# Optimization experiments

Measured on AMD Instinct MI355X. Metric: run time of the kernel, lower is better.

The kernel has to match this reference:

```python
import jax, jax.numpy as jnp
import numpy as np

DIM = 1024
NUM_HEADS = 16
HEAD_DIM = DIM // NUM_HEADS
SCALE = HEAD_DIM ** -0.5


def setup_inputs() -> dict:
    key = jax.random.key(0)
    k_x, k_wqkv, k_bqkv, k_wp, k_bp = jax.random.split(key, 5)
    B, C, D = 4, 1024, DIM
    x = jax.random.normal(k_x, (B, C, D), dtype=jnp.float32)
    # nn.Linear stores weight as (out, in); we keep (in, out) for x @ W
    w_qkv = jax.random.normal(k_wqkv, (D, 3 * D), dtype=jnp.float32) * (D ** -0.5)
    b_qkv = jax.random.normal(k_bqkv, (3 * D,), dtype=jnp.float32) * 0.02
    w_proj = jax.random.normal(k_wp, (D, D), dtype=jnp.float32) * (D ** -0.5)
    b_proj = jax.random.normal(k_bp, (D,), dtype=jnp.float32) * 0.02
    return {"x": x, "w_qkv": w_qkv, "b_qkv": b_qkv, "w_proj": w_proj, "b_proj": b_proj}


def reference(x, w_qkv, b_qkv, w_proj, b_proj):
    B, C, D = x.shape
    H, Hd = NUM_HEADS, HEAD_DIM
    qkv = x @ w_qkv + b_qkv                       # (B, C, 3D)
    qkv = qkv.reshape(B, C, 3, H, Hd)
    q = qkv[:, :, 0].transpose(0, 2, 1, 3)        # (B, H, C, Hd)
    k = qkv[:, :, 1].transpose(0, 2, 1, 3)
    v = qkv[:, :, 2].transpose(0, 2, 1, 3)
    attn = jnp.einsum('bhqd,bhkd->bhqk', q, k) * SCALE
    attn = jax.nn.softmax(attn, axis=-1)
    out = jnp.einsum('bhqk,bhkd->bhqd', attn, v)  # (B, H, C, Hd)
    out = out.transpose(0, 2, 1, 3).reshape(B, C, D)
    return out @ w_proj + b_proj
```

## Files before the change

kernel.cpp:

```cpp
#include <hip/hip_runtime.h>
#include <cstdint>

#define BB 4
#define CC 1024
#define DD 1024
#define HH 16
#define HD 64
#define NH3 3072

typedef __attribute__((ext_vector_type(8))) short short8;
typedef __attribute__((ext_vector_type(4))) float f32x4;

#define MFMA16(a, b, c) __builtin_amdgcn_mfma_f32_16x16x32_bf16(a, b, c, 0, 0, 0)
#define EXP2 __builtin_amdgcn_exp2f

__device__ __forceinline__ void glds16(const void* g, void* l) {
    __builtin_amdgcn_global_load_lds(
        (const __attribute__((address_space(1))) void*)g,
        (__attribute__((address_space(3))) void*)l, 16, 0, 0);
}

__device__ __forceinline__ ushort f2bf(float f) {
    union { float f; uint32_t u; } v; v.f = f;
    uint32_t r = v.u + 0x7FFF + ((v.u >> 16) & 1);
    return (ushort)(r >> 16);
}

__device__ __forceinline__ uint32_t pack2bf(float a, float b) {
    uint32_t ua = __float_as_uint(a), ub = __float_as_uint(b);
    ua += 0x7FFF + ((ua >> 16) & 1);
    ub += 0x7FFF + ((ub >> 16) & 1);
    return __builtin_amdgcn_perm(ua, ub, 0x03020706);
}

__global__ __launch_bounds__(256)
void prep_kernel(const float* __restrict__ x, ushort* __restrict__ xbf,
                 const float* __restrict__ wqkv, ushort* __restrict__ wqkvT,
                 const float* __restrict__ wprj, ushort* __restrict__ wprjT)
{
    __shared__ float Ts[64 * 65];
    const int blk = blockIdx.x;
    const int t = threadIdx.x;

    if (blk < 4096) {
        int i = blk * 256 + t;
        float4 v = ((const float4*)x)[i];
        ushort4 o;
        o.x = f2bf(v.x); o.y = f2bf(v.y); o.z = f2bf(v.z); o.w = f2bf(v.w);
        ((ushort4*)xbf)[i] = o;
        return;
    }

    const float* in; ushort* outp; int K, N, n0, k0;
    if (blk < 4864) {
        int bx = blk - 4096;
        in = wqkv; outp = wqkvT; K = DD; N = NH3;
        n0 = (bx % 48) * 64; k0 = (bx / 48) * 64;
    } else {
        int bx = blk - 4864;
        in = wprj; outp = wprjT; K = DD; N = DD;
        n0 = (bx % 16) * 64; k0 = (bx / 16) * 64;
    }
    #pragma unroll
    for (int i = 0; i < 16; ++i) {
        int idx = t + i * 256;
        int r = idx >> 6, c = idx & 63;
        Ts[r * 65 + c] = in[(size_t)(k0 + r) * N + n0 + c];
    }
    __syncthreads();
    #pragma unroll
    for (int i = 0; i < 16; ++i) {
        int idx = t + i * 256;
        int rr = idx >> 6, cc = idx & 63;
        outp[(size_t)(n0 + rr) * K + k0 + cc] = f2bf(Ts[cc * 65 + rr]);
    }
}

template<int MODE, int MT>
__global__ __launch_bounds__(256)
void gemm_bt(const ushort* __restrict__ A, const ushort* __restrict__ Bt,
             const float* __restrict__ bias, float* __restrict__ Cf,
             ushort* __restrict__ qb, ushort* __restrict__ kb, ushort* __restrict__ vtb,
             int M, int N, int K)
{
    constexpr int MI = MT / 32;
    __shared__ ushort As[3][MT * 32];
    __shared__ ushort Bs[3][128 * 32];

    const int tid = threadIdx.x;
    const int wid = tid >> 6, lane = tid & 63;
    const int quad = lane >> 4, l15 = lane & 15;
    const int m0 = blockIdx.y * MT, n0 = blockIdx.x * 128;
    const int wm = (wid >> 1) * (MT / 2), wn = (wid & 1) * 64;

    const int sr = lane >> 2;
    const int sc = lane & 3;

    const int ar0 = wid * (MT / 4) + sr;
    const int acg0 = sc ^ ((ar0 >> 1) & 3);
    const int acg1 = sc ^ (((ar0 + 16) >> 1) & 3);
    const ushort* Ar0 = A + (size_t)(m0 + ar0) * K + acg0 * 8;
    const ushort* Ar1 = A + (size_t)(m0 + ar0 + 16) * K + acg1 * 8;
    const int br0 = wid * 32 + sr;
    const int bcg0 = sc ^ ((br0 >> 1) & 3);
    const int bcg1 = sc ^ (((br0 + 16) >> 1) & 3);
    const ushort* Br0 = Bt + (size_t)(n0 + br0) * K + bcg0 * 8;
    const ushort* Br1 = Bt + (size_t)(n0 + br0 + 16) * K + bcg1 * 8;

    f32x4 acc[MI][4];
    #pragma unroll
    for (int i = 0; i < MI; ++i)
        #pragma unroll
        for (int j = 0; j < 4; ++j) acc[i][j] = (f32x4)(0.0f);

#define GSTAGE(kn, bidx) do { \
        glds16(Ar0 + (kn), &As[bidx][(wid * (MT / 4)) * 32]); \
        glds16(Br0 + (kn), &Bs[bidx][(wid * 32) * 32]); \
        if (MT == 128) glds16(Ar1 + (kn), &As[bidx][(wid * 32 + 16) * 32]); \
        glds16(Br1 + (kn), &Bs[bidx][(wid * 32 + 16) * 32]); } while (0)

    GSTAGE(0, 0);
    GSTAGE(32, 1);

    int cur = 0;
    for (int k0 = 0; k0 < K; k0 += 32) {
        if (k0 + 32 < K) {
            if (MT == 128)
                asm volatile("s_waitcnt vmcnt(4)\n\ts_barrier" ::: "memory");
            else
                asm volatile("s_waitcnt vmcnt(3)\n\ts_barrier" ::: "memory");
        } else {
            asm volatile("s_waitcnt vmcnt(0)\n\ts_barrier" ::: "memory");
        }
        if (k0 + 64 < K) {
            const int nb = (cur >= 1) ? cur - 1 : 2;
            GSTAGE(k0 + 64, nb);
        }

        short8 af[MI], bf[4];
        #pragma unroll
        for (int i = 0; i < MI; ++i) {
            int row = wm + i * 16 + l15;
            af[i] = *(const short8*)(&As[cur][row * 32 + (quad ^ ((row >> 1) & 3)) * 8]);
        }
        #pragma unroll
        for (int j = 0; j < 4; ++j) {
            int col = wn + j * 16 + l15;
            bf[j] = *(const short8*)(&Bs[cur][col * 32 + (quad ^ ((col >> 1) & 3)) * 8]);
        }
        #pragma unroll
        for (int i = 0; i < MI; ++i)
            #pragma unroll
            for (int j = 0; j < 4; ++j)
                acc[i][j] = MFMA16(af[i], bf[j], acc[i][j]);

        cur = (cur == 2) ? 0 : cur + 1;
    }
#undef GSTAGE

    if (MODE == 0) {
        #pragma unroll
        for (int i = 0; i < MI; ++i) {
            int row = m0 + wm + i * 16 + quad * 4;
            #pragma unroll
            for (int j = 0; j < 4; ++j) {
                int col = n0 + wn + j * 16 + l15;
                float bv = bias[col];
                #pragma unroll
                for (int r = 0; r < 4; ++r)
                    Cf[(size_t)(row + r) * N + col] = acc[i][j][r] + bv;
            }
        }
    } else {
        #pragma unroll
        for (int j = 0; j < 4; ++j) {
            int n = n0 + wn + j * 16 + l15;
            int three = n >> 10;
            int h = (n >> 6) & 15;
            int hd = n & 63;
            float scale = (three == 0) ? 0.1803368801f : 1.0f;
            float bv = bias[n];
            #pragma unroll
            for (int i = 0; i < MI; ++i) {
                int row = m0 + wm + i * 16 + quad * 4;
                #pragma unroll
                for (int r = 0; r < 4; ++r) {
                    int m = row + r;
                    int b = m >> 10, c = m & 1023;
                    ushort val = f2bf((acc[i][j][r] + bv) * scale);
                    if (three == 0)
                        qb[((size_t)((b * HH + h) * CC) + c) * HD + hd] = val;
                    else if (three == 1)
                        kb[((size_t)((b * HH + h) * CC) + c) * HD + hd] = val;
                    else
                        vtb[((size_t)((b * HH + h) * HD) + hd) * CC + c] = val;
                }
            }
        }
    }
}

__global__ __launch_bounds__(256)
void attn_mfma6(const ushort* __restrict__ qb, const ushort* __restrict__ kb,
                const ushort* __restrict__ vt, ushort* __restrict__ attnb)
{
    __shared__ ushort lds[2 * 4096 + 3 * 4096 + 2 * 9216];
    const uint K0 = 0, K1 = 4096;
    const uint V0 = 8192, V1 = 12288, V2 = 16384;
    const uint P0 = 20480, P1 = 29696;

    const int tid = threadIdx.x;
    const int wid = tid >> 6, lane = tid & 63;
    const int quad = lane >> 4, l15 = lane & 15;
    const int bh = blockIdx.x & 63;
    const int qt = blockIdx.x >> 6;
    const int q0 = qt * 128;
    const int b = bh >> 4, h = bh & 15;

    const ushort* Qp  = qb + ((size_t)bh * CC + q0) * HD;
    const ushort* Kp  = kb + (size_t)bh * CC * HD;
    const ushort* Vtp = vt + (size_t)bh * HD * CC;

    const int sr = lane >> 3;
    const int sc = lane & 7;

    short8 qf[2][2];
    #pragma unroll
    for (int q2 = 0; q2 < 2; ++q2) {
        int row = wid * 32 + q2 * 16 + l15;
        #pragma unroll
        for (int s = 0; s < 2; ++s)
            qf[q2][s] = *(const short8*)(Qp + (size_t)row * HD + (s * 4 + quad) * 8);
    }

    const int kr = wid * 16 + sr;
    const int cgA = sc ^ (kr & 7);
    const int cgB = sc ^ ((kr + 8) & 7);
    const ushort* Kr0 = Kp  + (size_t)kr * HD + cgA * 8;
    const ushort* Kr1 = Kp  + (size_t)(kr + 8) * HD + cgB * 8;
    const ushort* Vr0 = Vtp + (size_t)kr * CC + cgA * 8;
    const ushort* Vr1 = Vtp + (size_t)(kr + 8) * CC + cgB * 8;

    const uint stg0 = (wid * 16) * 64;
    const uint stg1 = (wid * 16 + 8) * 64;

    glds16(Kr0, lds + K0 + stg0);
    glds16(Kr1, lds + K0 + stg1);
    glds16(Vr0, lds + V0 + stg0);
    glds16(Vr1, lds + V0 + stg1);

    f32x4 oacc[2][4];
    #pragma unroll
    for (int q2 = 0; q2 < 2; ++q2)
        #pragma unroll
        for (int hb = 0; hb < 4; ++hb) oacc[q2][hb] = (f32x4)(0.0f);
    float lsum[2] = {0.0f, 0.0f};

    uint ksC = K0, ksN = K1;
    uint vsP = V2, vsC = V0, vsN = V1;
    uint psC = P0, psP = P1;

    for (int kt = 0; kt < 16; ++kt) {
        __syncthreads();
        if (kt < 15) {
            const int koff = (kt + 1) * 64;
            glds16(Kr0 + (size_t)koff * HD, lds + ksN + stg0);
            glds16(Kr1 + (size_t)koff * HD, lds + ksN + stg1);
            glds16(Vr0 + koff,              lds + vsN + stg0);
            glds16(Vr1 + koff,              lds + vsN + stg1);
        }

        if (kt > 0) {
            short8 vf[4][2];
            #pragma unroll
            for (int hb = 0; hb < 4; ++hb) {
                int hr = hb * 16 + l15;
                vf[hb][0] = *(const short8*)(lds + vsP + hr * 64 + ((quad ^ (hr & 7)) * 8));
                vf[hb][1] = *(const short8*)(lds + vsP + hr * 64 + (((4 + quad) ^ (hr & 7)) * 8));
            }
            #pragma unroll
            for (int q2 = 0; q2 < 2; ++q2) {
                int row = wid * 32 + q2 * 16 + l15;
                short8 pf0 = *(const short8*)(lds + psP + row * 72 + quad * 8);
                short8 pf1 = *(const short8*)(lds + psP + row * 72 + 32 + quad * 8);
                #pragma unroll
                for (int hb = 0; hb < 4; ++hb) {
                    oacc[q2][hb] = MFMA16(pf0, vf[hb][0], oacc[q2][hb]);
                    oacc[q2][hb] = MFMA16(pf1, vf[hb][1], oacc[q2][hb]);
                }
            }
        }

        #pragma unroll
        for (int kb2 = 0; kb2 < 4; ++kb2) {
            int krow = kb2 * 16 + l15;
            short8 kf0 = *(const short8*)(lds + ksC + krow * 64 + ((quad ^ (krow & 7)) * 8));
            short8 kf1 = *(const short8*)(lds + ksC + krow * 64 + (((4 + quad) ^ (krow & 7)) * 8));
            #pragma unroll
            for (int q2 = 0; q2 < 2; ++q2) {
                f32x4 st = (f32x4)(0.0f);
                st = MFMA16(kf0, qf[q2][0], st);
                st = MFMA16(kf1, qf[q2][1], st);
                float p0 = EXP2(st[0]);
                float p1 = EXP2(st[1]);
                float p2 = EXP2(st[2]);
                float p3 = EXP2(st[3]);
                lsum[q2] += (p0 + p1) + (p2 + p3);
                int row = wid * 32 + q2 * 16 + l15;
                *(uint2*)(lds + psC + row * 72 + kb2 * 16 + quad * 4) =
                    make_uint2(pack2bf(p0, p1), pack2bf(p2, p3));
            }
        }

        uint t = vsP; vsP = vsC; vsC = vsN; vsN = t;
        t = ksC; ksC = ksN; ksN = t;
        t = psP; psP = psC; psC = t;
    }

    {
        short8 vf[4][2];
        #pragma unroll
        for (int hb = 0; hb < 4; ++hb) {
            int hr = hb * 16 + l15;
            vf[hb][0] = *(const short8*)(lds + vsP + hr * 64 + ((quad ^ (hr & 7)) * 8));
            vf[hb][1] = *(const short8*)(lds + vsP + hr * 64 + (((4 + quad) ^ (hr & 7)) * 8));
        }
        #pragma unroll
        for (int q2 = 0; q2 < 2; ++q2) {
            int row = wid * 32 + q2 * 16 + l15;
            short8 pf0 = *(const short8*)(lds + psP + row * 72 + quad * 8);
            short8 pf1 = *(const short8*)(lds + psP + row * 72 + 32 + quad * 8);
            #pragma unroll
            for (int hb = 0; hb < 4; ++hb) {
                oacc[q2][hb] = MFMA16(pf0, vf[hb][0], oacc[q2][hb]);
                oacc[q2][hb] = MFMA16(pf1, vf[hb][1], oacc[q2][hb]);
            }
        }
    }

    #pragma unroll
    for (int q2 = 0; q2 < 2; ++q2) {
        lsum[q2] += __shfl_xor(lsum[q2], 16);
        lsum[q2] += __shfl_xor(lsum[q2], 32);
    }

    #pragma unroll
    for (int q2 = 0; q2 < 2; ++q2) {
        #pragma unroll
        for (int r = 0; r < 4; ++r) {
            float inv = 1.0f / __shfl(lsum[q2], (lane & 48) | (quad * 4 + r));
            int c = q0 + wid * 32 + q2 * 16 + quad * 4 + r;
            #pragma unroll
            for (int hb = 0; hb < 4; ++hb) {
                int d = h * 64 + hb * 16 + l15;
                attnb[((size_t)(b * CC + c)) * DD + d] = f2bf(oacc[q2][hb][r] * inv);
            }
        }
    }
}

extern "C" void kernel_launch(void* const* d_in, const int* in_sizes, int n_in,
                              void* d_out, int out_size, void* d_ws, size_t ws_size,
                              hipStream_t stream)
{
    (void)in_sizes; (void)n_in; (void)out_size; (void)ws_size;
    const float* x      = (const float*)d_in[0];
    const float* w_qkv  = (const float*)d_in[1];
    const float* b_qkv  = (const float*)d_in[2];
    const float* w_proj = (const float*)d_in[3];
    const float* b_proj = (const float*)d_in[4];
    float* out = (float*)d_out;

    ushort* p = (ushort*)d_ws;
    ushort* xbf   = p;  p += (size_t)4 * 1024 * 1024;
    ushort* wqkvT = p;  p += (size_t)3 * 1024 * 1024;
    ushort* wprjT = p;  p += (size_t)1 * 1024 * 1024;
    ushort* qbuf  = p;  p += (size_t)4 * 1024 * 1024;
    ushort* kbuf  = p;  p += (size_t)4 * 1024 * 1024;
    ushort* vtb   = p;  p += (size_t)4 * 1024 * 1024;
    ushort* attnb = p;  p += (size_t)4 * 1024 * 1024;

    prep_kernel<<<5120, 256, 0, stream>>>(x, xbf, w_qkv, wqkvT, w_proj, wprjT);

    gemm_bt<1, 128><<<dim3(NH3 / 128, (BB * CC) / 128), 256, 0, stream>>>(
        xbf, wqkvT, b_qkv, nullptr, qbuf, kbuf, vtb, BB * CC, NH3, DD);

    attn_mfma6<<<512, 256, 0, stream>>>(qbuf, kbuf, vtb, attnb);

    gemm_bt<0, 64><<<dim3(DD / 128, (BB * CC) / 64), 256, 0, stream>>>(
        attnb, wprjT, b_proj, out, nullptr, nullptr, nullptr, BB * CC, DD, DD);
}
```

Measured before the change: 176.4 us.

## Keep P in registers via shuffles and deepen K/V prefetch to two tiles

The attention kernel stops staging the softmax probabilities in LDS. It keeps the packed bf16 P values in registers and rebuilds the PV MFMA operand layout with cross-lane shuffles. K/V loading becomes a triple/quad-buffered pipeline that prefetches two tiles ahead, waiting with an explicit vmcnt plus barrier instead of __syncthreads, and MFMA sections get raised wave priority. This aims to remove LDS write/read traffic and hide global load latency, at the cost of more shuffle instructions and register pressure.

Result: no change. 178.8 us (+1.3%).

```diff
diff --git a/kernel.cpp b/kernel.cpp
--- a/kernel.cpp
+++ b/kernel.cpp
@@ -200,14 +200,26 @@
     }
 }
 
+__device__ __forceinline__ short8 pvfrag(const uint32_t pk0[2], const uint32_t pk1[2],
+                                         int quad, int l15) {
+    union { short8 s; uint32_t u[4]; } r;
+    #pragma unroll
+    for (int w = 0; w < 4; ++w) {
+        int src = ((quad & 1) * 2 + (w >> 1)) * 16 + l15;
+        uint32_t v0 = (uint32_t)__shfl((int)pk0[w & 1], src);
+        uint32_t v1 = (uint32_t)__shfl((int)pk1[w & 1], src);
+        r.u[w] = (quad < 2) ? v0 : v1;
+    }
+    return r.s;
+}
+
 __global__ __launch_bounds__(256)
-void attn_mfma6(const ushort* __restrict__ qb, const ushort* __restrict__ kb,
+void attn_mfma7(const ushort* __restrict__ qb, const ushort* __restrict__ kb,
                 const ushort* __restrict__ vt, ushort* __restrict__ attnb)
 {
-    __shared__ ushort lds[2 * 4096 + 3 * 4096 + 2 * 9216];
-    const uint K0 = 0, K1 = 4096;
-    const uint V0 = 8192, V1 = 12288, V2 = 16384;
-    const uint P0 = 20480, P1 = 29696;
+    __shared__ ushort lds[3 * 4096 + 4 * 4096];
+    const uint K0 = 0, K1 = 4096, K2 = 8192;
+    const uint V0 = 12288, V1 = 16384, V2 = 20480, V3 = 24576;
 
     const int tid = threadIdx.x;
     const int wid = tid >> 6, lane = tid & 63;
@@ -248,6 +260,10 @@
     glds16(Kr1, lds + K0 + stg1);
     glds16(Vr0, lds + V0 + stg0);
     glds16(Vr1, lds + V0 + stg1);
+    glds16(Kr0 + (size_t)64 * HD, lds + K1 + stg0);
+    glds16(Kr1 + (size_t)64 * HD, lds + K1 + stg1);
+    glds16(Vr0 + 64, lds + V1 + stg0);
+    glds16(Vr1 + 64, lds + V1 + stg1);
 
     f32x4 oacc[2][4];
     #pragma unroll
@@ -256,87 +272,85 @@
         for (int hb = 0; hb < 4; ++hb) oacc[q2][hb] = (f32x4)(0.0f);
     float lsum[2] = {0.0f, 0.0f};
 
-    uint ksC = K0, ksN = K1;
-    uint vsP = V2, vsC = V0, vsN = V1;
-    uint psC = P0, psP = P1;
-
-    for (int kt = 0; kt < 16; ++kt) {
-        __syncthreads();
-        if (kt < 15) {
-            const int koff = (kt + 1) * 64;
-            glds16(Kr0 + (size_t)koff * HD, lds + ksN + stg0);
-            glds16(Kr1 + (size_t)koff * HD, lds + ksN + stg1);
-            glds16(Vr0 + koff,              lds + vsN + stg0);
-            glds16(Vr1 + koff,              lds + vsN + stg1);
-        }
-
-        if (kt > 0) {
-            short8 vf[4][2];
-            #pragma unroll
-            for (int hb = 0; hb < 4; ++hb) {
-                int hr = hb * 16 + l15;
-                vf[hb][0] = *(const short8*)(lds + vsP + hr * 64 + ((quad ^ (hr & 7)) * 8));
-                vf[hb][1] = *(const short8*)(lds + vsP + hr * 64 + (((4 + quad) ^ (hr & 7)) * 8));
-            }
-            #pragma unroll
-            for (int q2 = 0; q2 < 2; ++q2) {
-                int row = wid * 32 + q2 * 16 + l15;
-                short8 pf0 = *(const short8*)(lds + psP + row * 72 + quad * 8);
-                short8 pf1 = *(const short8*)(lds + psP + row * 72 + 32 + quad * 8);
-                #pragma unroll
-                for (int hb = 0; hb < 4; ++hb) {
-                    oacc[q2][hb] = MFMA16(pf0, vf[hb][0], oacc[q2][hb]);
-                    oacc[q2][hb] = MFMA16(pf1, vf[hb][1], oacc[q2][hb]);
-                }
-            }
-        }
-
-        #pragma unroll
-        for (int kb2 = 0; kb2 < 4; ++kb2) {
-            int krow = kb2 * 16 + l15;
-            short8 kf0 = *(const short8*)(lds + ksC + krow * 64 + ((quad ^ (krow & 7)) * 8));
-            short8 kf1 = *(const short8*)(lds + ksC + krow * 64 + (((4 + quad) ^ (krow & 7)) * 8));
-            #pragma unroll
-            for (int q2 = 0; q2 < 2; ++q2) {
-                f32x4 st = (f32x4)(0.0f);
-                st = MFMA16(kf0, qf[q2][0], st);
-                st = MFMA16(kf1, qf[q2][1], st);
-                float p0 = EXP2(st[0]);
-                float p1 = EXP2(st[1]);
-                float p2 = EXP2(st[2]);
-                float p3 = EXP2(st[3]);
-                lsum[q2] += (p0 + p1) + (p2 + p3);
-                int row = wid * 32 + q2 * 16 + l15;
-                *(uint2*)(lds + psC + row * 72 + kb2 * 16 + quad * 4) =
-                    make_uint2(pack2bf(p0, p1), pack2bf(p2, p3));
-            }
-        }
-
-        uint t = vsP; vsP = vsC; vsC = vsN; vsN = t;
-        t = ksC; ksC = ksN; ksN = t;
-        t = psP; psP = psC; psC = t;
-    }
-
-    {
-        short8 vf[4][2];
-        #pragma unroll
-        for (int hb = 0; hb < 4; ++hb) {
-            int hr = hb * 16 + l15;
-            vf[hb][0] = *(const short8*)(lds + vsP + hr * 64 + ((quad ^ (hr & 7)) * 8));
-            vf[hb][1] = *(const short8*)(lds + vsP + hr * 64 + (((4 + quad) ^ (hr & 7)) * 8));
-        }
-        #pragma unroll
-        for (int q2 = 0; q2 < 2; ++q2) {
-            int row = wid * 32 + q2 * 16 + l15;
-            short8 pf0 = *(const short8*)(lds + psP + row * 72 + quad * 8);
-            short8 pf1 = *(const short8*)(lds + psP + row * 72 + 32 + quad * 8);
-            #pragma unroll
-            for (int hb = 0; hb < 4; ++hb) {
-                oacc[q2][hb] = MFMA16(pf0, vf[hb][0], oacc[q2][hb]);
-                oacc[q2][hb] = MFMA16(pf1, vf[hb][1], oacc[q2][hb]);
-            }
-        }
-    }
+    uint ksC = K0, ksN = K1, ksF = K2;
+    uint vsP = V3, vsC = V0, vsN = V1, vsF = V2;
+
+    uint32_t pkA[2][4][2], pkB[2][4][2];
+    #pragma unroll
+    for (int q2 = 0; q2 < 2; ++q2)
+        #pragma unroll
+        for (int kb2 = 0; kb2 < 4; ++kb2)
+            pkA[q2][kb2][0] = pkA[q2][kb2][1] = 0u;
+
+#define APV(PKP) do { \
+        short8 vf_[4][2]; \
+        _Pragma("unroll") \
+        for (int hb = 0; hb < 4; ++hb) { \
+            int hr = hb * 16 + l15; \
+            vf_[hb][0] = *(const short8*)(lds + vsP + hr * 64 + ((quad ^ (hr & 7)) * 8)); \
+            vf_[hb][1] = *(const short8*)(lds + vsP + hr * 64 + (((4 + quad) ^ (hr & 7)) * 8)); \
+        } \
+        short8 pf_[2][2]; \
+        _Pragma("unroll") \
+        for (int q2 = 0; q2 < 2; ++q2) { \
+            pf_[q2][0] = pvfrag(PKP[q2][0], PKP[q2][1], quad, l15); \
+            pf_[q2][1] = pvfrag(PKP[q2][2], PKP[q2][3], quad, l15); \
+        } \
+        __builtin_amdgcn_s_setprio(1); \
+        _Pragma("unroll") \
+        for (int q2 = 0; q2 < 2; ++q2) \
+            _Pragma("unroll") \
+            for (int hb = 0; hb < 4; ++hb) { \
+                oacc[q2][hb] = MFMA16(pf_[q2][0], vf_[hb][0], oacc[q2][hb]); \
+                oacc[q2][hb] = MFMA16(pf_[q2][1], vf_[hb][1], oacc[q2][hb]); \
+            } \
+        __builtin_amdgcn_s_setprio(0); \
+    } while (0)
+
+#define AITER(kt, PKP, PKC) do { \
+        if ((kt) < 15) asm volatile("s_waitcnt vmcnt(4)\n\ts_barrier" ::: "memory"); \
+        else           asm volatile("s_waitcnt vmcnt(0)\n\ts_barrier" ::: "memory"); \
+        if ((kt) < 14) {                      \
+            const int koff_ = ((kt) + 2) * 64; \
+            glds16(Kr0 + (size_t)koff_ * HD, lds + ksF + stg0); \
+            glds16(Kr1 + (size_t)koff_ * HD, lds + ksF + stg1); \
+            glds16(Vr0 + koff_,              lds + vsF + stg0); \
+            glds16(Vr1 + koff_,              lds + vsF + stg1); \
+        } \
+        if ((kt) > 0) APV(PKP); \
+         \
+        _Pragma("unroll") \
+        for (int kb2 = 0; kb2 < 4; ++kb2) { \
+            int krow_ = kb2 * 16 + l15; \
+            short8 kf0_ = *(const short8*)(lds + ksC + krow_ * 64 + ((quad ^ (krow_ & 7)) * 8)); \
+            short8 kf1_ = *(const short8*)(lds + ksC + krow_ * 64 + (((4 + quad) ^ (krow_ & 7)) * 8)); \
+            _Pragma("unroll") \
+            for (int q2 = 0; q2 < 2; ++q2) { \
+                f32x4 st_ = (f32x4)(0.0f); \
+                st_ = MFMA16(kf0_, qf[q2][0], st_); \
+                st_ = MFMA16(kf1_, qf[q2][1], st_); \
+                float p0_ = EXP2(st_[0]); \
+                float p1_ = EXP2(st_[1]); \
+                float p2_ = EXP2(st_[2]); \
+                float p3_ = EXP2(st_[3]); \
+                lsum[q2] += (p0_ + p1_) + (p2_ + p3_); \
+                PKC[q2][kb2][0] = pack2bf(p0_, p1_); \
+                PKC[q2][kb2][1] = pack2bf(p2_, p3_); \
+            } \
+        } \
+         \
+        uint t_ = ksC; ksC = ksN; ksN = ksF; ksF = t_; \
+        t_ = vsP; vsP = vsC; vsC = vsN; vsN = vsF; vsF = t_; \
+    } while (0)
+
+    for (int k2 = 0; k2 < 8; ++k2) {
+        AITER(2 * k2,     pkA, pkB);
+        AITER(2 * k2 + 1, pkB, pkA);
+    }
+
+    APV(pkA);
+#undef AITER
+#undef APV
 
     #pragma unroll
     for (int q2 = 0; q2 < 2; ++q2) {
@@ -385,7 +399,7 @@
     gemm_bt<1, 128><<<dim3(NH3 / 128, (BB * CC) / 128), 256, 0, stream>>>(
         xbf, wqkvT, b_qkv, nullptr, qbuf, kbuf, vtb, BB * CC, NH3, DD);
 
-    attn_mfma6<<<512, 256, 0, stream>>>(qbuf, kbuf, vtb, attnb);
+    attn_mfma7<<<512, 256, 0, stream>>>(qbuf, kbuf, vtb, attnb);
 
     gemm_bt<0, 64><<<dim3(DD / 128, (BB * CC) / 64), 256, 0, stream>>>(
         attnb, wprjT, b_proj, out, nullptr, nullptr, nullptr, BB * CC, DD, DD);
```
